# Kernel tuning notes

Hardware: AMD Instinct MI355X
Metric: run time of the kernel (lower is better)

## Reference

```python
import jax, jax.numpy as jnp
import numpy as np

N, E, M = 100000, 3200000, 1000000  # nodes, message edges, scored move edges
DIN, H = 128, 64


def setup_inputs() -> dict:
    key = jax.random.key(0)
    ks = jax.random.split(key, 20)
    rn = lambda k, shape, s=0.05: (jax.random.normal(k, shape, jnp.float32) * s)
    return {
        "x": jax.random.normal(ks[0], (N, DIN), jnp.float32),
        "edge_index": jax.random.randint(ks[1], (2, E), 0, N, jnp.int64),
        "move_edge_index": jax.random.randint(ks[2], (2, M), 0, N, jnp.int64),
        "lin1_w": rn(ks[3], (DIN, H)), "lin1_b": jnp.zeros((H,), jnp.float32),
        "lin2_w": rn(ks[4], (H, H)), "lin2_b": jnp.zeros((H,), jnp.float32),
        "conv1_wl": rn(ks[5], (H, H)), "conv1_bl": jnp.zeros((H,), jnp.float32),
        "conv1_wr": rn(ks[6], (H, H)),
        "conv2_wl": rn(ks[7], (H, H)), "conv2_bl": jnp.zeros((H,), jnp.float32),
        "conv2_wr": rn(ks[8], (H, H)),
        "mlp_w1": rn(ks[9], (2 * H, H)), "mlp_b1": jnp.zeros((H,), jnp.float32),
        "mlp_w2": rn(ks[10], (H, 1)), "mlp_b2": jnp.zeros((1,), jnp.float32),
    }


def reference(x, edge_index, move_edge_index,
              lin1_w, lin1_b, lin2_w, lin2_b,
              conv1_wl, conv1_bl, conv1_wr,
              conv2_wl, conv2_bl, conv2_wr,
              mlp_w1, mlp_b1, mlp_w2, mlp_b2):
    n = x.shape[0]
    src, dst = edge_index[0], edge_index[1]
    # mean-aggregation degrees (PyG SAGEConv default aggr='mean'; isolated nodes -> 0)
    deg = jax.ops.segment_sum(jnp.ones(src.shape, x.dtype), dst, num_segments=n)
    inv_deg = (jnp.where(deg > 0, 1.0 / jnp.maximum(deg, 1.0), 0.0))[:, None]

    def sage(h, wl, bl, wr):
        # out = W_l @ mean_j h_j + b_l + W_r @ h_i
        agg = jax.ops.segment_sum(h[src], dst, num_segments=n) * inv_deg
        return agg @ wl + bl + h @ wr

    h = jax.nn.relu(x @ lin1_w + lin1_b)
    h = jax.nn.relu(sage(h, conv1_wl, conv1_bl, conv1_wr))
    h = jax.nn.relu(h @ lin2_w + lin2_b)
    h = jax.nn.relu(sage(h, conv2_wl, conv2_bl, conv2_wr))

    # edge scoring: gather src/dst embeddings, concat, 2-layer MLP, tanh
    cat = jnp.concatenate([h[move_edge_index[0]], h[move_edge_index[1]]], axis=1)  # [M, 2H]
    logits = (jax.nn.relu(cat @ mlp_w1 + mlp_b1) @ mlp_w2 + mlp_b2).reshape(-1)
    return jnp.tanh(logits)
```

## Files before the change

### kernel.cpp

```cpp
#include <hip/hip_runtime.h>
#include <math.h>

#define MAXB 512
#define PART_CH 8192
#define PART_BS 1024

typedef _Float16 f16;
typedef __attribute__((ext_vector_type(2))) _Float16 f16x2;
typedef __attribute__((ext_vector_type(4))) _Float16 f16x4;
typedef __attribute__((ext_vector_type(8))) _Float16 f16x8;
typedef __attribute__((ext_vector_type(4))) float f32x4;

static __device__ __forceinline__ unsigned short f2h(float f) {
    f16 h = (f16)f; return *(unsigned short*)&h;
}

__global__ __launch_bounds__(PART_BS) void k_part(const int* __restrict__ src,
                                                  const int* __restrict__ dst,
                                                  int* __restrict__ bcur,
                                                  unsigned* __restrict__ bb,
                                                  int E, int shift, int CAP) {
    __shared__ int h[MAXB], base[MAXB];
    int b0 = blockIdx.x * PART_CH;
    int e1 = min(b0 + PART_CH, E);
    for (int i = threadIdx.x; i < MAXB; i += PART_BS) h[i] = 0;
    __syncthreads();
    for (int i = b0 + threadIdx.x; i < e1; i += PART_BS)
        atomicAdd(&h[dst[i] >> shift], 1);
    __syncthreads();
    for (int i = threadIdx.x; i < MAXB; i += PART_BS) {
        base[i] = h[i] ? atomicAdd(&bcur[i], h[i]) : 0;
        h[i] = 0;
    }
    __syncthreads();
    unsigned mask = (1u << shift) - 1u;
    for (int i = b0 + threadIdx.x; i < e1; i += PART_BS) {
        int d = dst[i];
        int b = d >> shift;
        int r = atomicAdd(&h[b], 1);
        unsigned p = (unsigned)base[b] + (unsigned)r;
        if (p < (unsigned)CAP)
            bb[(size_t)b * CAP + p] = ((unsigned)src[i] << shift) | ((unsigned)d & mask);
    }
}

__global__ __launch_bounds__(512) void k_bfill(const unsigned* __restrict__ bb,
                                               const int* __restrict__ bcur,
                                               int* __restrict__ row_st,
                                               int* __restrict__ row_en,
                                               float* __restrict__ inv_deg,
                                               int* __restrict__ csr,
                                               int N, int shift, int CAP) {
    __shared__ int deg[512], cur[512], s[512];
    int b = blockIdx.x;
    int t = threadIdx.x;
    int lo = b << shift;
    int hi = min(N, (b + 1) << shift);
    int nn = hi - lo;
    unsigned off = (unsigned)b * CAP;
    int cnt = min(bcur[b], CAP);
    unsigned mask = (1u << shift) - 1u;

    deg[t] = 0;
    __syncthreads();
    for (int i = t; i < cnt; i += 512)
        atomicAdd(&deg[bb[off + i] & mask], 1);
    __syncthreads();
    int d = deg[t];
    int pd = (d + 31) & ~31;
    s[t] = pd;
    __syncthreads();
    for (int o = 1; o < 512; o <<= 1) {
        int u = (t >= o) ? s[t - o] : 0;
        __syncthreads();
        s[t] += u;
        __syncthreads();
    }
    int excl = min(s[t] - pd, CAP);
    int pe = min(excl + pd, CAP);
    cur[t] = excl;
    if (t < nn) {
        row_st[lo + t] = (int)off + excl;
        row_en[lo + t] = (int)off + pe;
        inv_deg[lo + t] = d > 0 ? 1.0f / (float)d : 0.0f;
        for (int j = excl + d; j < pe; ++j) csr[off + j] = N;
    }
    __syncthreads();
    for (int i = t; i < cnt; i += 512) {
        unsigned w = bb[off + i];
        int dl = (int)(w & mask);
        int pos = atomicAdd(&cur[dl], 1);
        if (pos < CAP) csr[off + pos] = (int)(w >> shift);
    }
}

__global__ __launch_bounds__(256) void k_prep(
    const float* __restrict__ lin1_w, const float* __restrict__ c1_wl,
    const float* __restrict__ c1_wr, const float* __restrict__ lin2_w,
    const float* __restrict__ c2_wl, const float* __restrict__ c2_wr,
    const float* __restrict__ mlp_w1, const float* __restrict__ mlp_w2,
    unsigned short* __restrict__ Wt, int* __restrict__ bcur) {
    if (blockIdx.x == 0)
        for (int j = threadIdx.x; j < MAXB; j += 256) bcur[j] = 0;
    int i = blockIdx.x * 256 + threadIdx.x;
    for (; i < 36928; i += gridDim.x * 256) {
        float v;
        if (i < 8192)       { int j = i;         int n = j >> 7, k = j & 127; v = lin1_w[k * 64 + n]; }
        else if (i < 16384) { int j = i - 8192;  int n = j >> 7, k = j & 127;
                              v = (k < 64) ? c1_wl[k * 64 + n] : c1_wr[(k - 64) * 64 + n]; }
        else if (i < 20480) { int j = i - 16384; int n = j >> 6, k = j & 63;  v = lin2_w[k * 64 + n]; }
        else if (i < 28672) { int j = i - 20480; int n = j >> 7, k = j & 127;
                              v = (k < 64) ? c2_wl[k * 64 + n] : c2_wr[(k - 64) * 64 + n]; }
        else if (i < 32768) { int j = i - 28672; int n = j >> 6, k = j & 63;  v = mlp_w1[k * 64 + n]; }
        else if (i < 36864) { int j = i - 32768; int n = j >> 6, k = j & 63;  v = mlp_w1[(k + 64) * 64 + n]; }
        else                { v = mlp_w2[i - 36864]; }
        Wt[i] = f2h(v);
    }
}

__global__ __launch_bounds__(256) void k_gather_h(
    const _Float16* __restrict__ hh, const int* __restrict__ csr,
    const int* __restrict__ row_st, const int* __restrict__ row_en,
    const float* __restrict__ inv_deg, _Float16* __restrict__ out, int n) {
    int node = (blockIdx.x * 256 + (int)threadIdx.x) >> 6;
    if (node >= n) return;
    int lane = threadIdx.x & 63;
    int g = lane >> 3, sub = lane & 7;
    int base = row_st[node], end = row_en[node];
    float a[8] = {0.f, 0.f, 0.f, 0.f, 0.f, 0.f, 0.f, 0.f};
#if __has_builtin(__builtin_amdgcn_fdot2)
    const f16x2 one2 = {(f16)1.f, (f16)1.f};
#endif
    for (; base < end; base += 32) {
        int4 s4 = *(const int4*)&csr[base + 4 * g];
        int sidx[4] = {s4.x, s4.y, s4.z, s4.w};
        f16x8 u[4];
#pragma unroll
        for (int t = 0; t < 4; ++t)
            u[t] = *(const f16x8*)(hh + (((unsigned)sidx[t] << 6) + ((unsigned)sub << 3)));
#if __has_builtin(__builtin_amdgcn_fdot2)
#pragma unroll
        for (int t = 0; t < 4; t += 2)
#pragma unroll
            for (int j = 0; j < 8; ++j) {
                f16x2 v = {u[t][j], u[t + 1][j]};
                a[j] = __builtin_amdgcn_fdot2(v, one2, a[j], false);
            }
#else
#pragma unroll
        for (int t = 0; t < 4; ++t)
#pragma unroll
            for (int j = 0; j < 8; ++j) a[j] += (float)u[t][j];
#endif
    }
#pragma unroll
    for (int j = 0; j < 8; ++j) {
        a[j] += __shfl_xor(a[j], 8, 64);
        a[j] += __shfl_xor(a[j], 16, 64);
        a[j] += __shfl_xor(a[j], 32, 64);
    }
    if (g == 0) {
        float idv = inv_deg[node];
        f16x8 o;
#pragma unroll
        for (int j = 0; j < 8; ++j) o[j] = (f16)(a[j] * idv);
        *(f16x8*)(out + (((unsigned)node << 6) + ((unsigned)sub << 3))) = o;
    }
}

__global__ __launch_bounds__(256) void k_mm1(
    const float* __restrict__ x, const unsigned short* __restrict__ Wtg,
    const float* __restrict__ bias, unsigned short* __restrict__ outh, int n) {
    __shared__ alignas(16) unsigned short sW[64 * 136];
    const int tid = threadIdx.x;
    const int row0 = blockIdx.x * 64;
    if (blockIdx.x == 0 && tid < 8)
        ((uint4*)(outh + (size_t)n * 64))[tid] = (uint4){0, 0, 0, 0};
    for (int i = tid; i < 64 * 16; i += 256) {
        int nn = i >> 4, c = i & 15;
        *(uint4*)&sW[(nn * 17 + c) * 8] = *(const uint4*)&Wtg[i * 8];
    }
    __syncthreads();
    const int lane = tid & 63, w = tid >> 6;
    const int m = lane & 15, q = lane >> 4;
    const int gr = min(row0 + 16 * w + m, n - 1);
    const float* ar = x + (size_t)gr * 128;
    f32x4 acc[4];
#pragma unroll
    for (int c = 0; c < 4; ++c) acc[c] = (f32x4){0.f, 0.f, 0.f, 0.f};
#pragma unroll
    for (int kk = 0; kk < 4; ++kk) {
        float4 a0 = *(const float4*)(ar + kk * 32 + q * 8);
        float4 a1 = *(const float4*)(ar + kk * 32 + q * 8 + 4);
        f16x8 af;
        af[0] = (f16)a0.x; af[1] = (f16)a0.y; af[2] = (f16)a0.z; af[3] = (f16)a0.w;
        af[4] = (f16)a1.x; af[5] = (f16)a1.y; af[6] = (f16)a1.z; af[7] = (f16)a1.w;
#pragma unroll
        for (int c = 0; c < 4; ++c) {
            f16x8 bf = *(const f16x8*)&sW[((16 * c + m) * 17 + (kk * 4 + q)) * 8];
            acc[c] = __builtin_amdgcn_mfma_f32_16x16x32_f16(af, bf, acc[c], 0, 0, 0);
        }
    }
#pragma unroll
    for (int c = 0; c < 4; ++c) {
        int col = 16 * c + m;
        float bv = bias[col];
#pragma unroll
        for (int i = 0; i < 4; ++i) {
            int r = row0 + 16 * w + q * 4 + i;
            if (r < n) outh[(size_t)r * 64 + col] = f2h(fmaxf(acc[c][i] + bv, 0.f));
        }
    }
}

__global__ __launch_bounds__(256) void k_mm23(
    const unsigned short* __restrict__ aggH, const unsigned short* __restrict__ h1,
    const unsigned short* __restrict__ Wcg, const float* __restrict__ bl,
    const unsigned short* __restrict__ Wl2g, const float* __restrict__ b2,
    unsigned short* __restrict__ outh, int n) {
    __shared__ alignas(16) unsigned short sm[64 * 72 + 64 * 136];
    unsigned short* hA = sm;
    unsigned short* sW = sm + 64 * 72;
    const int tid = threadIdx.x;
    const int row0 = blockIdx.x * 64;
    for (int i = tid; i < 64 * 16; i += 256) {
        int nn = i >> 4, c = i & 15;
        *(uint4*)&sW[(nn * 17 + c) * 8] = *(const uint4*)&Wcg[i * 8];
    }
    __syncthreads();
    const int lane = tid & 63, w = tid >> 6;
    const int m = lane & 15, q = lane >> 4;
    const int gr = min(row0 + 16 * w + m, n - 1);
    f32x4 acc[4];
#pragma unroll
    for (int c = 0; c < 4; ++c) acc[c] = (f32x4){0.f, 0.f, 0.f, 0.f};
#pragma unroll
    for (int kk = 0; kk < 4; ++kk) {
        const unsigned short* ap = (kk < 2)
            ? (aggH + (size_t)gr * 64 + kk * 32 + q * 8)
            : (h1 + (size_t)gr * 64 + (kk - 2) * 32 + q * 8);
        f16x8 af = *(const f16x8*)ap;
#pragma unroll
        for (int c = 0; c < 4; ++c) {
            f16x8 bf = *(const f16x8*)&sW[((16 * c + m) * 17 + (kk * 4 + q)) * 8];
            acc[c] = __builtin_amdgcn_mfma_f32_16x16x32_f16(af, bf, acc[c], 0, 0, 0);
        }
    }
#pragma unroll
    for (int c = 0; c < 4; ++c) {
        int col = 16 * c + m;
        float bv = bl[col];
#pragma unroll
        for (int i = 0; i < 4; ++i)
            hA[(16 * w + q * 4 + i) * 72 + col] = f2h(fmaxf(acc[c][i] + bv, 0.f));
    }
    __syncthreads();
    for (int i = tid; i < 64 * 8; i += 256) {
        int nn = i >> 3, c = i & 7;
        *(uint4*)&sW[(nn * 9 + c) * 8] = *(const uint4*)&Wl2g[i * 8];
    }
    __syncthreads();
    f32x4 acc2[4];
#pragma unroll
    for (int c = 0; c < 4; ++c) acc2[c] = (f32x4){0.f, 0.f, 0.f, 0.f};
#pragma unroll
    for (int kk = 0; kk < 2; ++kk) {
        f16x8 af = *(const f16x8*)&hA[(16 * w + m) * 72 + kk * 32 + q * 8];
#pragma unroll
        for (int c = 0; c < 4; ++c) {
            f16x8 bf = *(const f16x8*)&sW[((16 * c + m) * 9 + (kk * 4 + q)) * 8];
            acc2[c] = __builtin_amdgcn_mfma_f32_16x16x32_f16(af, bf, acc2[c], 0, 0, 0);
        }
    }
#pragma unroll
    for (int c = 0; c < 4; ++c) {
        int col = 16 * c + m;
        float bv = b2[col];
#pragma unroll
        for (int i = 0; i < 4; ++i) {
            int r = row0 + 16 * w + q * 4 + i;
            if (r < n) outh[(size_t)r * 64 + col] = f2h(fmaxf(acc2[c][i] + bv, 0.f));
        }
    }
}

__global__ __launch_bounds__(256) void k_mm456(
    const unsigned short* __restrict__ aggH, const unsigned short* __restrict__ h3,
    const unsigned short* __restrict__ Wcg, const float* __restrict__ bl,
    const unsigned short* __restrict__ Wpg, const unsigned short* __restrict__ Wqg,
    const float* __restrict__ b1, unsigned short* __restrict__ Ph,
    unsigned short* __restrict__ Qh, int n) {
    __shared__ alignas(16) unsigned short sm[64 * 72 + 2 * 64 * 72];
    unsigned short* hA = sm;
    unsigned short* sW = sm + 64 * 72;
    const int tid = threadIdx.x;
    const int row0 = blockIdx.x * 64;
    for (int i = tid; i < 64 * 16; i += 256) {
        int nn = i >> 4, c = i & 15;
        *(uint4*)&sW[(nn * 17 + c) * 8] = *(const uint4*)&Wcg[i * 8];
    }
    __syncthreads();
    const int lane = tid & 63, w = tid >> 6;
    const int m = lane & 15, q = lane >> 4;
    const int gr = min(row0 + 16 * w + m, n - 1);
    f32x4 acc[4];
#pragma unroll
    for (int c = 0; c < 4; ++c) acc[c] = (f32x4){0.f, 0.f, 0.f, 0.f};
#pragma unroll
    for (int kk = 0; kk < 4; ++kk) {
        const unsigned short* ap = (kk < 2)
            ? (aggH + (size_t)gr * 64 + kk * 32 + q * 8)
            : (h3 + (size_t)gr * 64 + (kk - 2) * 32 + q * 8);
        f16x8 af = *(const f16x8*)ap;
#pragma unroll
        for (int c = 0; c < 4; ++c) {
            f16x8 bf = *(const f16x8*)&sW[((16 * c + m) * 17 + (kk * 4 + q)) * 8];
            acc[c] = __builtin_amdgcn_mfma_f32_16x16x32_f16(af, bf, acc[c], 0, 0, 0);
        }
    }
#pragma unroll
    for (int c = 0; c < 4; ++c) {
        int col = 16 * c + m;
        float bv = bl[col];
#pragma unroll
        for (int i = 0; i < 4; ++i)
            hA[(16 * w + q * 4 + i) * 72 + col] = f2h(fmaxf(acc[c][i] + bv, 0.f));
    }
    __syncthreads();
    for (int i = tid; i < 64 * 8; i += 256) {
        int nn = i >> 3, c = i & 7;
        *(uint4*)&sW[(nn * 9 + c) * 8] = *(const uint4*)&Wpg[i * 8];
        *(uint4*)&sW[4608 + (nn * 9 + c) * 8] = *(const uint4*)&Wqg[i * 8];
    }
    __syncthreads();
    f32x4 accP[4], accQ[4];
#pragma unroll
    for (int c = 0; c < 4; ++c) {
        accP[c] = (f32x4){0.f, 0.f, 0.f, 0.f};
        accQ[c] = (f32x4){0.f, 0.f, 0.f, 0.f};
    }
#pragma unroll
    for (int kk = 0; kk < 2; ++kk) {
        f16x8 af = *(const f16x8*)&hA[(16 * w + m) * 72 + kk * 32 + q * 8];
#pragma unroll
        for (int c = 0; c < 4; ++c) {
            f16x8 bp = *(const f16x8*)&sW[((16 * c + m) * 9 + (kk * 4 + q)) * 8];
            f16x8 bq = *(const f16x8*)&sW[4608 + ((16 * c + m) * 9 + (kk * 4 + q)) * 8];
            accP[c] = __builtin_amdgcn_mfma_f32_16x16x32_f16(af, bp, accP[c], 0, 0, 0);
            accQ[c] = __builtin_amdgcn_mfma_f32_16x16x32_f16(af, bq, accQ[c], 0, 0, 0);
        }
    }
#pragma unroll
    for (int c = 0; c < 4; ++c) {
        int col = 16 * c + m;
        float bv = b1[col];
#pragma unroll
        for (int i = 0; i < 4; ++i) {
            int r = row0 + 16 * w + q * 4 + i;
            if (r < n) {
                Ph[(size_t)r * 64 + col] = f2h(accP[c][i] + bv);
                Qh[(size_t)r * 64 + col] = f2h(accQ[c][i]);
            }
        }
    }
}

__global__ __launch_bounds__(256) void k_score_h(
    const _Float16* __restrict__ P, const _Float16* __restrict__ Q,
    const int* __restrict__ msrc, const int* __restrict__ mdst,
    const _Float16* __restrict__ w2h, const float* __restrict__ b2,
    float* __restrict__ out, int M) {
    int gid = blockIdx.x * 256 + threadIdx.x;
    int e = gid >> 3;
    if (e >= M) return;
    int l = gid & 7;
    int s = msrc[e], d = mdst[e];
    f16x8 p = *(const f16x8*)(P + (((unsigned)s << 6) + ((unsigned)l << 3)));
    f16x8 q = *(const f16x8*)(Q + (((unsigned)d << 6) + ((unsigned)l << 3)));
    f16x8 w = *(const f16x8*)(w2h + ((unsigned)l << 3));
    f16x8 u = p + q;
    f16x8 z = {(f16)0, (f16)0, (f16)0, (f16)0, (f16)0, (f16)0, (f16)0, (f16)0};
    u = __builtin_elementwise_max(u, z);
    float partial;
#if __has_builtin(__builtin_amdgcn_fdot2)
    f16x2 u01 = {u[0], u[1]}, u23 = {u[2], u[3]}, u45 = {u[4], u[5]}, u67 = {u[6], u[7]};
    f16x2 w01 = {w[0], w[1]}, w23 = {w[2], w[3]}, w45 = {w[4], w[5]}, w67 = {w[6], w[7]};
    partial = __builtin_amdgcn_fdot2(u01, w01,
              __builtin_amdgcn_fdot2(u23, w23,
              __builtin_amdgcn_fdot2(u45, w45,
              __builtin_amdgcn_fdot2(u67, w67, 0.f, false), false), false), false);
#else
    partial = 0.f;
#pragma unroll
    for (int i = 0; i < 8; ++i) partial += (float)u[i] * (float)w[i];
#endif
    partial += __shfl_xor(partial, 1, 8);
    partial += __shfl_xor(partial, 2, 8);
    partial += __shfl_xor(partial, 4, 8);
    if (l == 0) {
        float xx = partial + b2[0];
        float t = __expf(2.f * xx);
        out[e] = (t - 1.f) / (t + 1.f);
    }
}

extern "C" void kernel_launch(void* const* d_in, const int* in_sizes, int n_in,
                              void* d_out, int out_size, void* d_ws, size_t ws_size,
                              hipStream_t stream) {
    const float* x      = (const float*)d_in[0];
    const int*   ei     = (const int*)d_in[1];
    const int*   mei    = (const int*)d_in[2];
    const float* lin1_w = (const float*)d_in[3];
    const float* lin1_b = (const float*)d_in[4];
    const float* lin2_w = (const float*)d_in[5];
    const float* lin2_b = (const float*)d_in[6];
    const float* c1_wl  = (const float*)d_in[7];
    const float* c1_bl  = (const float*)d_in[8];
    const float* c1_wr  = (const float*)d_in[9];
    const float* c2_wl  = (const float*)d_in[10];
    const float* c2_bl  = (const float*)d_in[11];
    const float* c2_wr  = (const float*)d_in[12];
    const float* mlp_w1 = (const float*)d_in[13];
    const float* mlp_b1 = (const float*)d_in[14];
    const float* mlp_w2 = (const float*)d_in[15];
    const float* mlp_b2 = (const float*)d_in[16];

    const int N = in_sizes[0] / 128;
    const int E = in_sizes[1] / 2;
    const int M = in_sizes[2] / 2;
    const int* src  = ei;
    const int* dstE = ei + E;
    const int* msrc = mei;
    const int* mdst = mei + M;

    int shift = 8;
    while ((((N - 1) >> shift) + 1) > MAXB) ++shift;
    const int nbuckets = ((N - 1) >> shift) + 1;
    long long avg = (((long long)E << shift) / N) + 1;
    int CAP = (int)((2 * avg + 2047) & ~1023LL);

    const size_t N64 = (size_t)N * 64;
    unsigned short* Hh   = (unsigned short*)d_ws;
    unsigned short* aggH = Hh + N64 + 64;
    unsigned short* Qh   = aggH + N64;
    float* inv_deg = (float*)(Qh + N64);
    int*   row_st  = (int*)(inv_deg + N);
    int*   row_en  = row_st + N;
    int*   bcur    = row_en + N;
    unsigned short* Wt = (unsigned short*)(bcur + MAXB);
    int*   csr     = (int*)(Wt + 36928 + 32);
    unsigned* bb   = (unsigned*)Hh;
    float* outf = (float*)d_out;

    const int nbN = (N + 63) / 64;
    const int nbM = (int)(((long long)M * 8 + 255) / 256);
    const int nbG = (int)(((long long)N * 64 + 255) / 256);
    const int nbP = (E + PART_CH - 1) / PART_CH;

    k_prep<<<64, 256, 0, stream>>>(lin1_w, c1_wl, c1_wr, lin2_w, c2_wl, c2_wr,
                                   mlp_w1, mlp_w2, Wt, bcur);
    k_part<<<nbP, PART_BS, 0, stream>>>(src, dstE, bcur, bb, E, shift, CAP);
    k_bfill<<<nbuckets, 512, 0, stream>>>(bb, bcur, row_st, row_en,
                                          inv_deg, csr, N, shift, CAP);

    k_mm1<<<nbN, 256, 0, stream>>>(x, Wt + 0, lin1_b, Hh, N);

    k_gather_h<<<nbG, 256, 0, stream>>>((const _Float16*)Hh, csr, row_st, row_en,
                                        inv_deg, (_Float16*)aggH, N);
    k_mm23<<<nbN, 256, 0, stream>>>(aggH, Hh, Wt + 8192, c1_bl,
                                    Wt + 16384, lin2_b, Hh, N);

    k_gather_h<<<nbG, 256, 0, stream>>>((const _Float16*)Hh, csr, row_st, row_en,
                                        inv_deg, (_Float16*)aggH, N);
    k_mm456<<<nbN, 256, 0, stream>>>(aggH, Hh, Wt + 20480, c2_bl,
                                     Wt + 28672, Wt + 32768, mlp_b1,
                                     Hh, Qh, N);

    k_score_h<<<nbM, 256, 0, stream>>>((const _Float16*)Hh, (const _Float16*)Qh,
                                       msrc, mdst, (const _Float16*)(Wt + 36864),
                                       mlp_b2, outf, M);
}
```

Measured before the change: 389.3 us.

## Partition edges into per-block bucket slots in one pass, and unroll gather by 64

The edge partition becomes a single pass. Each block writes into fixed-capacity private slots per bucket, and the histogram pass and the global atomic reservation on bucket cursors are gone. k_bfill then reads each bucket's slots and masks them with the per-block counts. The neighbor gather also processes 64 CSR entries per iteration instead of 32, putting more loads in flight. The risks are that a block's slot can silently overflow CAPB and drop edges on skewed inputs, and that bfill scans padded slots.

```diff
diff --git a/kernel.cpp b/kernel.cpp
--- a/kernel.cpp
+++ b/kernel.cpp
@@ -2,8 +2,8 @@
 #include <math.h>
 
 #define MAXB 512
-#define PART_CH 8192
 #define PART_BS 1024
+#define CAPB 256
 
 typedef _Float16 f16;
 typedef __attribute__((ext_vector_type(2))) _Float16 f16x2;
@@ -17,54 +17,72 @@
 
 __global__ __launch_bounds__(PART_BS) void k_part(const int* __restrict__ src,
                                                   const int* __restrict__ dst,
-                                                  int* __restrict__ bcur,
                                                   unsigned* __restrict__ bb,
-                                                  int E, int shift, int CAP) {
-    __shared__ int h[MAXB], base[MAXB];
-    int b0 = blockIdx.x * PART_CH;
-    int e1 = min(b0 + PART_CH, E);
+                                                  int* __restrict__ cnt,
+                                                  int E, int shift, int pcap,
+                                                  int nblk, int nb) {
+    __shared__ int h[MAXB];
+    const int blk = blockIdx.x;
+    const int b0 = blk * pcap;
+    const int e1 = min(b0 + pcap, E);
     for (int i = threadIdx.x; i < MAXB; i += PART_BS) h[i] = 0;
     __syncthreads();
-    for (int i = b0 + threadIdx.x; i < e1; i += PART_BS)
-        atomicAdd(&h[dst[i] >> shift], 1);
-    __syncthreads();
-    for (int i = threadIdx.x; i < MAXB; i += PART_BS) {
-        base[i] = h[i] ? atomicAdd(&bcur[i], h[i]) : 0;
-        h[i] = 0;
-    }
-    __syncthreads();
-    unsigned mask = (1u << shift) - 1u;
-    for (int i = b0 + threadIdx.x; i < e1; i += PART_BS) {
-        int d = dst[i];
-        int b = d >> shift;
-        int r = atomicAdd(&h[b], 1);
-        unsigned p = (unsigned)base[b] + (unsigned)r;
-        if (p < (unsigned)CAP)
-            bb[(size_t)b * CAP + p] = ((unsigned)src[i] << shift) | ((unsigned)d & mask);
-    }
+    const unsigned mask = (1u << shift) - 1u;
+    for (int pos = b0 + (int)threadIdx.x * 8; pos < e1; pos += PART_BS * 8) {
+        if (pos + 8 <= e1) {
+            int4 d0 = *(const int4*)(dst + pos), d1 = *(const int4*)(dst + pos + 4);
+            int4 s0 = *(const int4*)(src + pos), s1 = *(const int4*)(src + pos + 4);
+            int dd[8] = {d0.x, d0.y, d0.z, d0.w, d1.x, d1.y, d1.z, d1.w};
+            int ss[8] = {s0.x, s0.y, s0.z, s0.w, s1.x, s1.y, s1.z, s1.w};
+#pragma unroll
+            for (int k = 0; k < 8; ++k) {
+                int b = dd[k] >> shift;
+                int r = atomicAdd(&h[b], 1);
+                if (r < CAPB)
+                    bb[((size_t)b * nblk + blk) * CAPB + r] =
+                        ((unsigned)ss[k] << shift) | ((unsigned)dd[k] & mask);
+            }
+        } else {
+            for (int k = 0; pos + k < e1; ++k) {
+                int d = dst[pos + k];
+                int b = d >> shift;
+                int r = atomicAdd(&h[b], 1);
+                if (r < CAPB)
+                    bb[((size_t)b * nblk + blk) * CAPB + r] =
+                        ((unsigned)src[pos + k] << shift) | ((unsigned)d & mask);
+            }
+        }
+    }
+    __syncthreads();
+    for (int i = threadIdx.x; i < nb; i += PART_BS)
+        cnt[(size_t)i * nblk + blk] = min(h[i], CAPB);
 }
 
 __global__ __launch_bounds__(512) void k_bfill(const unsigned* __restrict__ bb,
-                                               const int* __restrict__ bcur,
+                                               const int* __restrict__ cnt,
                                                int* __restrict__ row_st,
                                                int* __restrict__ row_en,
                                                float* __restrict__ inv_deg,
                                                int* __restrict__ csr,
-                                               int N, int shift, int CAP) {
+                                               int N, int shift, int CAP, int nblk) {
     __shared__ int deg[512], cur[512], s[512];
+    __shared__ int scnt[1024];
     int b = blockIdx.x;
     int t = threadIdx.x;
     int lo = b << shift;
     int hi = min(N, (b + 1) << shift);
     int nn = hi - lo;
     unsigned off = (unsigned)b * CAP;
-    int cnt = min(bcur[b], CAP);
     unsigned mask = (1u << shift) - 1u;
-
+    const unsigned* seg = bb + (size_t)b * nblk * CAPB;
+
+    for (int i = t; i < nblk; i += 512) scnt[i] = cnt[(size_t)b * nblk + i];
     deg[t] = 0;
     __syncthreads();
-    for (int i = t; i < cnt; i += 512)
-        atomicAdd(&deg[bb[off + i] & mask], 1);
+    const int tot = nblk * CAPB;
+    for (int i = t; i < tot; i += 512)
+        if ((i & (CAPB - 1)) < scnt[i >> 8])
+            atomicAdd(&deg[seg[i] & mask], 1);
     __syncthreads();
     int d = deg[t];
     int pd = (d + 31) & ~31;
@@ -86,12 +104,13 @@
         for (int j = excl + d; j < pe; ++j) csr[off + j] = N;
     }
     __syncthreads();
-    for (int i = t; i < cnt; i += 512) {
-        unsigned w = bb[off + i];
-        int dl = (int)(w & mask);
-        int pos = atomicAdd(&cur[dl], 1);
-        if (pos < CAP) csr[off + pos] = (int)(w >> shift);
-    }
+    for (int i = t; i < tot; i += 512)
+        if ((i & (CAPB - 1)) < scnt[i >> 8]) {
+            unsigned w = seg[i];
+            int dl = (int)(w & mask);
+            int pos = atomicAdd(&cur[dl], 1);
+            if (pos < CAP) csr[off + pos] = (int)(w >> shift);
+        }
 }
 
 __global__ __launch_bounds__(256) void k_prep(
@@ -99,9 +118,7 @@
     const float* __restrict__ c1_wr, const float* __restrict__ lin2_w,
     const float* __restrict__ c2_wl, const float* __restrict__ c2_wr,
     const float* __restrict__ mlp_w1, const float* __restrict__ mlp_w2,
-    unsigned short* __restrict__ Wt, int* __restrict__ bcur) {
-    if (blockIdx.x == 0)
-        for (int j = threadIdx.x; j < MAXB; j += 256) bcur[j] = 0;
+    unsigned short* __restrict__ Wt) {
     int i = blockIdx.x * 256 + threadIdx.x;
     for (; i < 36928; i += gridDim.x * 256) {
         float v;
@@ -131,9 +148,32 @@
 #if __has_builtin(__builtin_amdgcn_fdot2)
     const f16x2 one2 = {(f16)1.f, (f16)1.f};
 #endif
-    for (; base < end; base += 32) {
-        int4 s4 = *(const int4*)&csr[base + 4 * g];
-        int sidx[4] = {s4.x, s4.y, s4.z, s4.w};
+    for (; base + 64 <= end; base += 64) {
+        int4 sA = *(const int4*)&csr[base + 4 * g];
+        int4 sB = *(const int4*)&csr[base + 32 + 4 * g];
+        int sidx[8] = {sA.x, sA.y, sA.z, sA.w, sB.x, sB.y, sB.z, sB.w};
+        f16x8 u[8];
+#pragma unroll
+        for (int t = 0; t < 8; ++t)
+            u[t] = *(const f16x8*)(hh + (((unsigned)sidx[t] << 6) + ((unsigned)sub << 3)));
+#if __has_builtin(__builtin_amdgcn_fdot2)
+#pragma unroll
+        for (int t = 0; t < 8; t += 2)
+#pragma unroll
+            for (int j = 0; j < 8; ++j) {
+                f16x2 v = {u[t][j], u[t + 1][j]};
+                a[j] = __builtin_amdgcn_fdot2(v, one2, a[j], false);
+            }
+#else
+#pragma unroll
+        for (int t = 0; t < 8; ++t)
+#pragma unroll
+            for (int j = 0; j < 8; ++j) a[j] += (float)u[t][j];
+#endif
+    }
+    if (base < end) {
+        int4 sA = *(const int4*)&csr[base + 4 * g];
+        int sidx[4] = {sA.x, sA.y, sA.z, sA.w};
         f16x8 u[4];
 #pragma unroll
         for (int t = 0; t < 4; ++t)
@@ -440,14 +480,22 @@
     int CAP = (int)((2 * avg + 2047) & ~1023LL);
 
     const size_t N64 = (size_t)N * 64;
+    const size_t aliasBytes = (3 * N64 + 64) * 2;
+    int pcap = 32768;
+    int nblk = (E + pcap - 1) / pcap;
+    while ((size_t)nblk * nbuckets * CAPB * 4 > aliasBytes || nblk > 1024) {
+        pcap <<= 1;
+        nblk = (E + pcap - 1) / pcap;
+    }
+
     unsigned short* Hh   = (unsigned short*)d_ws;
     unsigned short* aggH = Hh + N64 + 64;
     unsigned short* Qh   = aggH + N64;
     float* inv_deg = (float*)(Qh + N64);
     int*   row_st  = (int*)(inv_deg + N);
     int*   row_en  = row_st + N;
-    int*   bcur    = row_en + N;
-    unsigned short* Wt = (unsigned short*)(bcur + MAXB);
+    int*   cnt     = row_en + N;
+    unsigned short* Wt = (unsigned short*)(cnt + (size_t)nbuckets * nblk);
     int*   csr     = (int*)(Wt + 36928 + 32);
     unsigned* bb   = (unsigned*)Hh;
     float* outf = (float*)d_out;
@@ -455,13 +503,13 @@
     const int nbN = (N + 63) / 64;
     const int nbM = (int)(((long long)M * 8 + 255) / 256);
     const int nbG = (int)(((long long)N * 64 + 255) / 256);
-    const int nbP = (E + PART_CH - 1) / PART_CH;
 
     k_prep<<<64, 256, 0, stream>>>(lin1_w, c1_wl, c1_wr, lin2_w, c2_wl, c2_wr,
-                                   mlp_w1, mlp_w2, Wt, bcur);
-    k_part<<<nbP, PART_BS, 0, stream>>>(src, dstE, bcur, bb, E, shift, CAP);
-    k_bfill<<<nbuckets, 512, 0, stream>>>(bb, bcur, row_st, row_en,
-                                          inv_deg, csr, N, shift, CAP);
+                                   mlp_w1, mlp_w2, Wt);
+    k_part<<<nblk, PART_BS, 0, stream>>>(src, dstE, bb, cnt, E, shift, pcap,
+                                         nblk, nbuckets);
+    k_bfill<<<nbuckets, 512, 0, stream>>>(bb, cnt, row_st, row_en,
+                                          inv_deg, csr, N, shift, CAP, nblk);
 
     k_mm1<<<nbN, 256, 0, stream>>>(x, Wt + 0, lin1_b, Hh, N);
 
```

New measurement: 412.3 us. 5.9% more time.
